# Optimization experiments

Hardware: AMD Instinct MI355X
Metric: run time of the kernel (lower is better)

Reference implementation:

```python
import jax, jax.numpy as jnp
import numpy as np

N = 20000      # nodes
E = 320000     # directed edges (before self-loops)
IN, HID, HEADS, OUT = 512, 256, 4, 256
NEG_SLOPE = 0.2  # PyG GATConv default


def setup_inputs() -> dict:
    key = jax.random.key(0)
    ks = jax.random.split(key, 10)
    x = jax.random.normal(ks[0], (N, IN), jnp.float32)
    edge_index = jax.random.randint(ks[1], (2, E), 0, N, jnp.int32)
    W1 = jax.random.normal(ks[2], (IN, HEADS * HID), jnp.float32) / np.sqrt(IN).astype(np.float32)
    att_src1 = jax.random.normal(ks[3], (HEADS, HID), jnp.float32) * 0.1
    att_dst1 = jax.random.normal(ks[4], (HEADS, HID), jnp.float32) * 0.1
    b1 = jnp.zeros((HEADS * HID,), jnp.float32)
    W2 = jax.random.normal(ks[5], (HEADS * HID, OUT), jnp.float32) / np.sqrt(HEADS * HID).astype(np.float32)
    att_src2 = jax.random.normal(ks[6], (1, OUT), jnp.float32) * 0.1
    att_dst2 = jax.random.normal(ks[7], (1, OUT), jnp.float32) * 0.1
    b2 = jnp.zeros((OUT,), jnp.float32)
    return {"x": x, "edge_index": edge_index, "W1": W1, "att_src1": att_src1,
            "att_dst1": att_dst1, "b1": b1, "W2": W2, "att_src2": att_src2,
            "att_dst2": att_dst2, "b2": b2}


def _segment_softmax(logits, seg, num_segments):
    # softmax over edges grouped by destination node (per head)
    m = jax.ops.segment_max(logits, seg, num_segments=num_segments)
    ex = jnp.exp(logits - m[seg])
    s = jax.ops.segment_sum(ex, seg, num_segments=num_segments)
    return ex / (s[seg] + 1e-16)


def _gat_conv(x, src, dst, W, att_src, att_dst, bias, heads, ch, num_nodes, concat):
    # PyG GATConv: h = W x (per head); alpha_e = softmax_dst(LeakyReLU(a_s.h_src + a_d.h_dst))
    h = (x @ W).reshape(num_nodes, heads, ch)          # [N,H,C]
    a_s = (h * att_src).sum(-1)                        # [N,H]
    a_d = (h * att_dst).sum(-1)                        # [N,H]
    logits = jax.nn.leaky_relu(a_s[src] + a_d[dst], NEG_SLOPE)   # [E,H]
    alpha = _segment_softmax(logits, dst, num_nodes)             # [E,H]
    msg = h[src] * alpha[:, :, None]                             # [E,H,C]
    out = jax.ops.segment_sum(msg, dst, num_segments=num_nodes)  # [N,H,C]
    out = out.reshape(num_nodes, heads * ch) if concat else out.mean(axis=1)
    return out + bias


def reference(x, edge_index, W1, att_src1, att_dst1, b1, W2, att_src2, att_dst2, b2):
    # add self-loops (PyG default add_self_loops=True)
    loop = jnp.arange(N, dtype=edge_index.dtype)
    src = jnp.concatenate([edge_index[0], loop])
    dst = jnp.concatenate([edge_index[1], loop])
    h = jax.nn.elu(_gat_conv(x, src, dst, W1, att_src1, att_dst1, b1, HEADS, HID, N, True))
    return _gat_conv(h, src, dst, W2, att_src2, att_dst2, b2, 1, OUT, N, False)
```

## Files before the change

kernel.cpp:

```cpp
#include <hip/hip_runtime.h>
#include <hip/hip_bf16.h>
#include <cfloat>
#include <math.h>

#define N_NODES 20000
#define M_PAD   20096
#define N_EDGES 320000
#define TOT_E   (N_EDGES + N_NODES)
#define EPAD    512
#define PS      (TOT_E + EPAD)
#define IN_F    512
#define HID     256
#define HEADS   4
#define OUT_F   256
#define H1DIM   (HEADS * HID)
#define NEG_SLOPE 0.2f

typedef __attribute__((ext_vector_type(8))) __bf16 bf16x8;
typedef __attribute__((ext_vector_type(4))) __bf16 bf16x4;
typedef __attribute__((ext_vector_type(4))) float f32x4;

__device__ __forceinline__ float lrelu(float x) { return x >= 0.f ? x : NEG_SLOPE * x; }
__device__ __forceinline__ float elu_lite(float x) { return x > 0.f ? x : __expf(x) - 1.f; }

__global__ void k_count(const int* __restrict__ ei, int* __restrict__ deg) {
  int e = blockIdx.x * 256 + threadIdx.x;
  if (e >= TOT_E) return;
  int dst = (e < N_EDGES) ? ei[N_EDGES + e] : (e - N_EDGES);
  atomicAdd(&deg[dst], 1);
}

__global__ void k_scan(const int* __restrict__ deg, int* __restrict__ off) {
  __shared__ int part[256];
  int tid = threadIdx.x;
  const int chunk = (N_NODES + 255) / 256;
  int s0 = tid * chunk;
  int s1 = s0 + chunk; if (s1 > N_NODES) s1 = N_NODES; if (s0 > N_NODES) s0 = N_NODES;
  int s = 0;
  for (int i = s0; i < s1; ++i) s += deg[i];
  part[tid] = s;
  __syncthreads();
  for (int d = 1; d < 256; d <<= 1) {
    int v = (tid >= d) ? part[tid - d] : 0;
    __syncthreads();
    part[tid] += v;
    __syncthreads();
  }
  int run = (tid == 0) ? 0 : part[tid - 1];
  for (int i = s0; i < s1; ++i) { off[i] = run; run += deg[i]; }
  if (tid == 255) off[N_NODES] = run;
}

__global__ void k_fill(const int* __restrict__ ei, const int* __restrict__ off,
                       int* __restrict__ cur, int* __restrict__ csr_src) {
  int e = blockIdx.x * 256 + threadIdx.x;
  if (e >= TOT_E) return;
  int src, dst;
  if (e < N_EDGES) { src = ei[e]; dst = ei[N_EDGES + e]; }
  else             { src = dst = e - N_EDGES; }
  int pos = atomicAdd(&cur[dst], 1);
  csr_src[off[dst] + pos] = src;
}

__global__ void k_f2b(const float* __restrict__ in, __bf16* __restrict__ out, int n4) {
  int i = blockIdx.x * 256 + threadIdx.x;
  if (i >= n4) return;
  float4 v = ((const float4*)in)[i];
  bf16x4 o = { (__bf16)v.x, (__bf16)v.y, (__bf16)v.z, (__bf16)v.w };
  ((bf16x4*)out)[i] = o;
}

__global__ void k_tr_f2b(const float* __restrict__ in, __bf16* __restrict__ out,
                         int R, int Cc) {
  __shared__ float tile[32][33];
  int c0 = blockIdx.x * 32, r0 = blockIdx.y * 32;
  int tx = threadIdx.x & 31, ty = threadIdx.x >> 5;
  for (int rr = ty; rr < 32; rr += 8)
    tile[rr][tx] = in[(size_t)(r0 + rr) * Cc + c0 + tx];
  __syncthreads();
  for (int rr = ty; rr < 32; rr += 8)
    out[(size_t)(c0 + rr) * R + r0 + tx] = (__bf16)tile[tx][rr];
}

__global__ __launch_bounds__(256) void k_gemm_bf16(
    const __bf16* __restrict__ A,
    const __bf16* __restrict__ Bt,
    __bf16* __restrict__ Cb,
    int M, int N, int K)
{
  __shared__ char lds[32768];
  char* As = lds;
  char* Bs = lds + 16384;

  const int t = threadIdx.x;
  const int lane = t & 63;
  const int wid = t >> 6;
  const int wm = wid >> 1, wn = wid & 1;
  const int row0 = blockIdx.y * 128;
  const int col0 = blockIdx.x * 128;

  f32x4 acc[4][4];
#pragma unroll
  for (int i = 0; i < 4; ++i)
#pragma unroll
    for (int j = 0; j < 4; ++j) acc[i][j] = (f32x4){0.f, 0.f, 0.f, 0.f};

  for (int k0 = 0; k0 < K; k0 += 64) {
#pragma unroll
    for (int i = 0; i < 4; ++i) {
      int j = i * 256 + t;
      int r = j >> 3;
      int cc = (j & 7) ^ (r & 7);
      const __bf16* gp = A + (size_t)(row0 + r) * K + k0 + cc * 8;
      __builtin_amdgcn_global_load_lds(
          (const __attribute__((address_space(1))) void*)gp,
          (__attribute__((address_space(3))) void*)(As + j * 16), 16, 0, 0);
    }
#pragma unroll
    for (int i = 0; i < 4; ++i) {
      int j = i * 256 + t;
      int r = j >> 3;
      int cc = (j & 7) ^ (r & 7);
      const __bf16* gp = Bt + (size_t)(col0 + r) * K + k0 + cc * 8;
      __builtin_amdgcn_global_load_lds(
          (const __attribute__((address_space(1))) void*)gp,
          (__attribute__((address_space(3))) void*)(Bs + j * 16), 16, 0, 0);
    }
    __syncthreads();

#pragma unroll
    for (int ks = 0; ks < 2; ++ks) {
      bf16x8 af[4], bfr[4];
#pragma unroll
      for (int i = 0; i < 4; ++i) {
        int rA = wm * 64 + i * 16 + (lane & 15);
        int chA = (ks * 4 + (lane >> 4)) ^ (rA & 7);
        af[i] = *(const bf16x8*)(As + rA * 128 + chA * 16);
        int rB = wn * 64 + i * 16 + (lane & 15);
        int chB = (ks * 4 + (lane >> 4)) ^ (rB & 7);
        bfr[i] = *(const bf16x8*)(Bs + rB * 128 + chB * 16);
      }
#pragma unroll
      for (int i = 0; i < 4; ++i)
#pragma unroll
        for (int jn = 0; jn < 4; ++jn)
          acc[i][jn] = __builtin_amdgcn_mfma_f32_16x16x32_bf16(
              af[i], bfr[jn], acc[i][jn], 0, 0, 0);
    }
    __syncthreads();
  }

#pragma unroll
  for (int i = 0; i < 4; ++i) {
    int growb = row0 + wm * 64 + i * 16 + (lane >> 4) * 4;
#pragma unroll
    for (int jn = 0; jn < 4; ++jn) {
      int gcol = col0 + wn * 64 + jn * 16 + (lane & 15);
#pragma unroll
      for (int r = 0; r < 4; ++r) {
        int grow = growb + r;
        if (grow < M) Cb[(size_t)grow * N + gcol] = (__bf16)acc[i][jn][r];
      }
    }
  }
}

__global__ void k_attn1(const __bf16* __restrict__ h1b, const float* __restrict__ att_s,
                        const float* __restrict__ att_d, float* __restrict__ as,
                        float* __restrict__ ad) {
  int n = blockIdx.x;
  int t = threadIdx.x;
  int head = t >> 6, lane = t & 63;
  bf16x4 hv = *(const bf16x4*)(h1b + (size_t)n * H1DIM + t * 4);
  float4 sv = *(const float4*)(att_s + t * 4);
  float4 dv = *(const float4*)(att_d + t * 4);
  float h0 = (float)hv[0], h1 = (float)hv[1], h2 = (float)hv[2], h3 = (float)hv[3];
  float ss = h0 * sv.x + h1 * sv.y + h2 * sv.z + h3 * sv.w;
  float sd = h0 * dv.x + h1 * dv.y + h2 * dv.z + h3 * dv.w;
#pragma unroll
  for (int d = 32; d; d >>= 1) { ss += __shfl_xor(ss, d); sd += __shfl_xor(sd, d); }
  if (lane == 0) { as[n * HEADS + head] = ss; ad[n * HEADS + head] = sd; }
}

__global__ void k_attn2(const __bf16* __restrict__ h2b, const float* __restrict__ att_s,
                        const float* __restrict__ att_d, float* __restrict__ as,
                        float* __restrict__ ad) {
  int n = blockIdx.x;
  int lane = threadIdx.x;
  bf16x4 hv = *(const bf16x4*)(h2b + (size_t)n * OUT_F + lane * 4);
  float4 sv = *(const float4*)(att_s + lane * 4);
  float4 dv = *(const float4*)(att_d + lane * 4);
  float h0 = (float)hv[0], h1 = (float)hv[1], h2 = (float)hv[2], h3 = (float)hv[3];
  float ss = h0 * sv.x + h1 * sv.y + h2 * sv.z + h3 * sv.w;
  float sd = h0 * dv.x + h1 * dv.y + h2 * dv.z + h3 * dv.w;
#pragma unroll
  for (int d = 32; d; d >>= 1) { ss += __shfl_xor(ss, d); sd += __shfl_xor(sd, d); }
  if (lane == 0) { as[n] = ss; ad[n] = sd; }
}

__global__ void k_w1(const int* __restrict__ off, const int* __restrict__ csr,
                     const float* __restrict__ as, const float* __restrict__ ad,
                     float* __restrict__ wnP, float* __restrict__ inv) {
  int n = blockIdx.x;
  int lane = threadIdx.x;
  int beg = off[n], end = off[n + 1];
  float4 adv = *(const float4*)&ad[n * 4];
  float p0 = 0.f, p1 = 0.f, p2 = 0.f, p3 = 0.f;
  for (int p = beg + lane; p < end; p += 64) {
    int s = csr[p];
    float4 av = *(const float4*)&as[s * 4];
    float w0 = __expf(lrelu(av.x + adv.x));
    float w1 = __expf(lrelu(av.y + adv.y));
    float w2 = __expf(lrelu(av.z + adv.z));
    float w3 = __expf(lrelu(av.w + adv.w));
    p0 += w0; p1 += w1; p2 += w2; p3 += w3;
    wnP[p] = w0;
    wnP[PS + p] = w1;
    wnP[2 * PS + p] = w2;
    wnP[3 * PS + p] = w3;
  }
#pragma unroll
  for (int d = 32; d; d >>= 1) {
    p0 += __shfl_xor(p0, d); p1 += __shfl_xor(p1, d);
    p2 += __shfl_xor(p2, d); p3 += __shfl_xor(p3, d);
  }
  if (lane == 0) {
    float4 iv = {1.f / (p0 + 1e-16f), 1.f / (p1 + 1e-16f),
                 1.f / (p2 + 1e-16f), 1.f / (p3 + 1e-16f)};
    *(float4*)&inv[n * 4] = iv;
  }
}

__global__ void k_w2(const int* __restrict__ off, const int* __restrict__ csr,
                     const float* __restrict__ as, const float* __restrict__ ad,
                     float* __restrict__ wn, float* __restrict__ inv) {
  int n = blockIdx.x;
  int lane = threadIdx.x;
  int beg = off[n], end = off[n + 1];
  float adv = ad[n];
  float ps = 0.f;
  for (int p = beg + lane; p < end; p += 64) {
    int s = csr[p];
    float w = __expf(lrelu(as[s] + adv));
    wn[p] = w;
    ps += w;
  }
#pragma unroll
  for (int d = 32; d; d >>= 1) ps += __shfl_xor(ps, d);
  if (lane == 0) inv[n] = 1.f / (ps + 1e-16f);
}

__global__ __launch_bounds__(256) void k_gather1(
    const int* __restrict__ off, const int* __restrict__ csr,
    const __bf16* __restrict__ h1b, const float* __restrict__ wnP,
    const float* __restrict__ inv, const float* __restrict__ b1,
    __bf16* __restrict__ heluB) {
  int bid = blockIdx.x;
  int slice = bid & 7;
  int head = slice >> 1;
  int cb = slice * 128;
  int w = threadIdx.x >> 6, lane = threadIdx.x & 63;
  int g = lane >> 4;
  int cg = lane & 15;
  int n = (bid >> 3) * 16 + w * 4 + g;
  int beg = off[n], end = off[n + 1];
  int deg = end - beg;
  int itmax = deg;
  itmax = max(itmax, __shfl_xor(itmax, 16));
  itmax = max(itmax, __shfl_xor(itmax, 32));

  float acc[8] = {0.f, 0.f, 0.f, 0.f, 0.f, 0.f, 0.f, 0.f};
  const __bf16* hb = h1b + cb + cg * 8;
  const float* wp = wnP + (size_t)head * PS;
#pragma unroll 2
  for (int i = 0; i < itmax; ++i) {
    int e = beg + i;
    bool v = (i < deg);
    int s = v ? csr[e] : 0;
    float wv = v ? wp[e] : 0.f;
    uint4 u = *(const uint4*)(hb + (size_t)s * H1DIM);
    acc[0] = fmaf(wv, __uint_as_float(u.x << 16), acc[0]);
    acc[1] = fmaf(wv, __uint_as_float(u.x & 0xffff0000u), acc[1]);
    acc[2] = fmaf(wv, __uint_as_float(u.y << 16), acc[2]);
    acc[3] = fmaf(wv, __uint_as_float(u.y & 0xffff0000u), acc[3]);
    acc[4] = fmaf(wv, __uint_as_float(u.z << 16), acc[4]);
    acc[5] = fmaf(wv, __uint_as_float(u.z & 0xffff0000u), acc[5]);
    acc[6] = fmaf(wv, __uint_as_float(u.w << 16), acc[6]);
    acc[7] = fmaf(wv, __uint_as_float(u.w & 0xffff0000u), acc[7]);
  }

  float iv = inv[n * 4 + head];
  float4 bv0 = *(const float4*)(b1 + cb + cg * 8);
  float4 bv1 = *(const float4*)(b1 + cb + cg * 8 + 4);
  float bb[8] = {bv0.x, bv0.y, bv0.z, bv0.w, bv1.x, bv1.y, bv1.z, bv1.w};
  bf16x8 o;
#pragma unroll
  for (int k = 0; k < 8; ++k) {
    float v = acc[k] * iv + bb[k];
    o[k] = (__bf16)elu_lite(v);
  }
  *(bf16x8*)(heluB + (size_t)n * H1DIM + cb + cg * 8) = o;
}

__global__ __launch_bounds__(256) void k_gather2(
    const int* __restrict__ off, const int* __restrict__ csr,
    const __bf16* __restrict__ h2b, const float* __restrict__ wn,
    const float* __restrict__ inv, const float* __restrict__ b2,
    float* __restrict__ out) {
  int bid = blockIdx.x;
  int slice = bid & 3;
  int cb = slice * 64;
  int w = threadIdx.x >> 6, lane = threadIdx.x & 63;
  int g = lane >> 3;
  int cg = lane & 7;
  int n = (bid >> 2) * 32 + w * 8 + g;
  int beg = off[n], end = off[n + 1];
  int deg = end - beg;
  int itmax = deg;
  itmax = max(itmax, __shfl_xor(itmax, 8));
  itmax = max(itmax, __shfl_xor(itmax, 16));
  itmax = max(itmax, __shfl_xor(itmax, 32));

  float acc[8] = {0.f, 0.f, 0.f, 0.f, 0.f, 0.f, 0.f, 0.f};
  const __bf16* hb = h2b + cb + cg * 8;
#pragma unroll 2
  for (int i = 0; i < itmax; ++i) {
    int e = beg + i;
    bool v = (i < deg);
    int s = v ? csr[e] : 0;
    float wv = v ? wn[e] : 0.f;
    uint4 u = *(const uint4*)(hb + (size_t)s * OUT_F);
    acc[0] = fmaf(wv, __uint_as_float(u.x << 16), acc[0]);
    acc[1] = fmaf(wv, __uint_as_float(u.x & 0xffff0000u), acc[1]);
    acc[2] = fmaf(wv, __uint_as_float(u.y << 16), acc[2]);
    acc[3] = fmaf(wv, __uint_as_float(u.y & 0xffff0000u), acc[3]);
    acc[4] = fmaf(wv, __uint_as_float(u.z << 16), acc[4]);
    acc[5] = fmaf(wv, __uint_as_float(u.z & 0xffff0000u), acc[5]);
    acc[6] = fmaf(wv, __uint_as_float(u.w << 16), acc[6]);
    acc[7] = fmaf(wv, __uint_as_float(u.w & 0xffff0000u), acc[7]);
  }

  float iv = inv[n];
  float4 bv0 = *(const float4*)(b2 + cb + cg * 8);
  float4 bv1 = *(const float4*)(b2 + cb + cg * 8 + 4);
  float* op = out + (size_t)n * OUT_F + cb + cg * 8;
  float4 o0 = {acc[0] * iv + bv0.x, acc[1] * iv + bv0.y,
               acc[2] * iv + bv0.z, acc[3] * iv + bv0.w};
  float4 o1 = {acc[4] * iv + bv1.x, acc[5] * iv + bv1.y,
               acc[6] * iv + bv1.z, acc[7] * iv + bv1.w};
  *(float4*)op = o0;
  *(float4*)(op + 4) = o1;
}

extern "C" void kernel_launch(void* const* d_in, const int* in_sizes, int n_in,
                              void* d_out, int out_size, void* d_ws, size_t ws_size,
                              hipStream_t stream) {
  const float* x      = (const float*)d_in[0];
  const int*   ei     = (const int*)d_in[1];
  const float* W1     = (const float*)d_in[2];
  const float* att_s1 = (const float*)d_in[3];
  const float* att_d1 = (const float*)d_in[4];
  const float* b1     = (const float*)d_in[5];
  const float* W2     = (const float*)d_in[6];
  const float* att_s2 = (const float*)d_in[7];
  const float* att_d2 = (const float*)d_in[8];
  const float* b2     = (const float*)d_in[9];
  float* out = (float*)d_out;

  char* w = (char*)d_ws;
  auto alloc = [&](size_t bytes) {
    char* p = w;
    w += (bytes + 255) & ~(size_t)255;
    return p;
  };
  int*    deg   = (int*)alloc((size_t)N_NODES * 4);
  int*    off   = (int*)alloc((size_t)(N_NODES + 1) * 4);
  int*    cur   = (int*)alloc((size_t)N_NODES * 4);
  int*    csr   = (int*)alloc((size_t)PS * 4);
  float*  as1   = (float*)alloc((size_t)N_NODES * HEADS * 4);
  float*  ad1   = (float*)alloc((size_t)N_NODES * HEADS * 4);
  float*  as2   = (float*)alloc((size_t)N_NODES * 4);
  float*  ad2   = (float*)alloc((size_t)N_NODES * 4);
  float*  wnP   = (float*)alloc((size_t)PS * HEADS * 4);
  float*  inv1  = (float*)alloc((size_t)N_NODES * HEADS * 4);
  float*  wn2   = (float*)alloc((size_t)PS * 4);
  float*  inv2  = (float*)alloc((size_t)N_NODES * 4);
  __bf16* xb    = (__bf16*)alloc((size_t)M_PAD * IN_F * 2);
  __bf16* w1t   = (__bf16*)alloc((size_t)H1DIM * IN_F * 2);
  __bf16* w2t   = (__bf16*)alloc((size_t)OUT_F * H1DIM * 2);
  __bf16* h1b   = (__bf16*)alloc((size_t)M_PAD * H1DIM * 2);
  __bf16* heluB = (__bf16*)alloc((size_t)M_PAD * H1DIM * 2);
  __bf16* h2b   = (__bf16*)alloc((size_t)M_PAD * OUT_F * 2);
  if ((size_t)(w - (char*)d_ws) > ws_size) return;

  hipMemsetAsync(deg, 0, (size_t)N_NODES * 4, stream);
  hipMemsetAsync(cur, 0, (size_t)N_NODES * 4, stream);
  hipMemsetAsync(csr + TOT_E, 0, (size_t)EPAD * 4, stream);

  k_count<<<(TOT_E + 255) / 256, 256, 0, stream>>>(ei, deg);
  k_scan<<<1, 256, 0, stream>>>(deg, off);
  k_fill<<<(TOT_E + 255) / 256, 256, 0, stream>>>(ei, off, cur, csr);

  int n4 = N_NODES * IN_F / 4;
  k_f2b<<<(n4 + 255) / 256, 256, 0, stream>>>(x, xb, n4);
  k_tr_f2b<<<dim3(H1DIM / 32, IN_F / 32), 256, 0, stream>>>(W1, w1t, IN_F, H1DIM);
  k_tr_f2b<<<dim3(OUT_F / 32, H1DIM / 32), 256, 0, stream>>>(W2, w2t, H1DIM, OUT_F);

  k_gemm_bf16<<<dim3(H1DIM / 128, M_PAD / 128), 256, 0, stream>>>(
      xb, w1t, h1b, N_NODES, H1DIM, IN_F);
  k_attn1<<<N_NODES, 256, 0, stream>>>(h1b, att_s1, att_d1, as1, ad1);
  k_w1<<<N_NODES, 64, 0, stream>>>(off, csr, as1, ad1, wnP, inv1);
  k_gather1<<<(N_NODES / 16) * 8, 256, 0, stream>>>(off, csr, h1b, wnP, inv1, b1, heluB);

  k_gemm_bf16<<<dim3(OUT_F / 128, M_PAD / 128), 256, 0, stream>>>(
      heluB, w2t, h2b, N_NODES, OUT_F, H1DIM);
  k_attn2<<<N_NODES, 64, 0, stream>>>(h2b, att_s2, att_d2, as2, ad2);
  k_w2<<<N_NODES, 64, 0, stream>>>(off, csr, as2, ad2, wn2, inv2);
  k_gather2<<<(N_NODES / 32) * 4, 256, 0, stream>>>(off, csr, h2b, wn2, inv2, b2, out);
}
```

Measured before the change: 303.6 us.

## Fuse attention-logit dot products into GEMM epilogue and split edges across gather lanes

```diff
diff --git a/kernel.cpp b/kernel.cpp
--- a/kernel.cpp
+++ b/kernel.cpp
@@ -86,6 +86,8 @@
     const __bf16* __restrict__ A,
     const __bf16* __restrict__ Bt,
     __bf16* __restrict__ Cb,
+    const float* __restrict__ attS, const float* __restrict__ attD,
+    float* __restrict__ asO, float* __restrict__ adO, int hstride,
     int M, int N, int K)
 {
   __shared__ char lds[32768];
@@ -163,39 +165,39 @@
       }
     }
   }
-}
-
-__global__ void k_attn1(const __bf16* __restrict__ h1b, const float* __restrict__ att_s,
-                        const float* __restrict__ att_d, float* __restrict__ as,
-                        float* __restrict__ ad) {
-  int n = blockIdx.x;
-  int t = threadIdx.x;
-  int head = t >> 6, lane = t & 63;
-  bf16x4 hv = *(const bf16x4*)(h1b + (size_t)n * H1DIM + t * 4);
-  float4 sv = *(const float4*)(att_s + t * 4);
-  float4 dv = *(const float4*)(att_d + t * 4);
-  float h0 = (float)hv[0], h1 = (float)hv[1], h2 = (float)hv[2], h3 = (float)hv[3];
-  float ss = h0 * sv.x + h1 * sv.y + h2 * sv.z + h3 * sv.w;
-  float sd = h0 * dv.x + h1 * dv.y + h2 * dv.z + h3 * dv.w;
-#pragma unroll
-  for (int d = 32; d; d >>= 1) { ss += __shfl_xor(ss, d); sd += __shfl_xor(sd, d); }
-  if (lane == 0) { as[n * HEADS + head] = ss; ad[n * HEADS + head] = sd; }
-}
-
-__global__ void k_attn2(const __bf16* __restrict__ h2b, const float* __restrict__ att_s,
-                        const float* __restrict__ att_d, float* __restrict__ as,
-                        float* __restrict__ ad) {
-  int n = blockIdx.x;
-  int lane = threadIdx.x;
-  bf16x4 hv = *(const bf16x4*)(h2b + (size_t)n * OUT_F + lane * 4);
-  float4 sv = *(const float4*)(att_s + lane * 4);
-  float4 dv = *(const float4*)(att_d + lane * 4);
-  float h0 = (float)hv[0], h1 = (float)hv[1], h2 = (float)hv[2], h3 = (float)hv[3];
-  float ss = h0 * sv.x + h1 * sv.y + h2 * sv.z + h3 * sv.w;
-  float sd = h0 * dv.x + h1 * dv.y + h2 * dv.z + h3 * dv.w;
-#pragma unroll
-  for (int d = 32; d; d >>= 1) { ss += __shfl_xor(ss, d); sd += __shfl_xor(sd, d); }
-  if (lane == 0) { as[n] = ss; ad[n] = sd; }
+
+  int head = (col0 + wn * 64) >> 8;
+  float sv[4], dv[4];
+#pragma unroll
+  for (int jn = 0; jn < 4; ++jn) {
+    int c = col0 + wn * 64 + jn * 16 + (lane & 15);
+    sv[jn] = attS[c];
+    dv[jn] = attD[c];
+  }
+#pragma unroll
+  for (int i = 0; i < 4; ++i) {
+#pragma unroll
+    for (int r = 0; r < 4; ++r) {
+      float pa = 0.f, pd = 0.f;
+#pragma unroll
+      for (int jn = 0; jn < 4; ++jn) {
+        pa = fmaf(acc[i][jn][r], sv[jn], pa);
+        pd = fmaf(acc[i][jn][r], dv[jn], pd);
+      }
+#pragma unroll
+      for (int d = 1; d < 16; d <<= 1) {
+        pa += __shfl_xor(pa, d);
+        pd += __shfl_xor(pd, d);
+      }
+      if ((lane & 15) == 0) {
+        int grow = row0 + wm * 64 + i * 16 + (lane >> 4) * 4 + r;
+        if (grow < M) {
+          atomicAdd(&asO[(size_t)grow * hstride + head], pa);
+          atomicAdd(&adO[(size_t)grow * hstride + head], pd);
+        }
+      }
+    }
+  }
 }
 
 __global__ void k_w1(const int* __restrict__ off, const int* __restrict__ csr,
@@ -260,22 +262,20 @@
   int head = slice >> 1;
   int cb = slice * 128;
   int w = threadIdx.x >> 6, lane = threadIdx.x & 63;
-  int g = lane >> 4;
+  int sub = lane >> 4;
   int cg = lane & 15;
-  int n = (bid >> 3) * 16 + w * 4 + g;
+  int n = (bid >> 3) * 4 + w;
   int beg = off[n], end = off[n + 1];
   int deg = end - beg;
-  int itmax = deg;
-  itmax = max(itmax, __shfl_xor(itmax, 16));
-  itmax = max(itmax, __shfl_xor(itmax, 32));
+  int it = (deg + 3) >> 2;
 
   float acc[8] = {0.f, 0.f, 0.f, 0.f, 0.f, 0.f, 0.f, 0.f};
   const __bf16* hb = h1b + cb + cg * 8;
   const float* wp = wnP + (size_t)head * PS;
 #pragma unroll 2
-  for (int i = 0; i < itmax; ++i) {
-    int e = beg + i;
-    bool v = (i < deg);
+  for (int i = 0; i < it; ++i) {
+    int e = beg + i * 4 + sub;
+    bool v = (e < end);
     int s = v ? csr[e] : 0;
     float wv = v ? wp[e] : 0.f;
     uint4 u = *(const uint4*)(hb + (size_t)s * H1DIM);
@@ -288,18 +288,24 @@
     acc[6] = fmaf(wv, __uint_as_float(u.w << 16), acc[6]);
     acc[7] = fmaf(wv, __uint_as_float(u.w & 0xffff0000u), acc[7]);
   }
-
-  float iv = inv[n * 4 + head];
-  float4 bv0 = *(const float4*)(b1 + cb + cg * 8);
-  float4 bv1 = *(const float4*)(b1 + cb + cg * 8 + 4);
-  float bb[8] = {bv0.x, bv0.y, bv0.z, bv0.w, bv1.x, bv1.y, bv1.z, bv1.w};
-  bf16x8 o;
 #pragma unroll
   for (int k = 0; k < 8; ++k) {
-    float v = acc[k] * iv + bb[k];
-    o[k] = (__bf16)elu_lite(v);
-  }
-  *(bf16x8*)(heluB + (size_t)n * H1DIM + cb + cg * 8) = o;
+    acc[k] += __shfl_xor(acc[k], 16);
+    acc[k] += __shfl_xor(acc[k], 32);
+  }
+  if (sub == 0) {
+    float iv = inv[n * 4 + head];
+    float4 bv0 = *(const float4*)(b1 + cb + cg * 8);
+    float4 bv1 = *(const float4*)(b1 + cb + cg * 8 + 4);
+    float bb[8] = {bv0.x, bv0.y, bv0.z, bv0.w, bv1.x, bv1.y, bv1.z, bv1.w};
+    bf16x8 o;
+#pragma unroll
+    for (int k = 0; k < 8; ++k) {
+      float v = acc[k] * iv + bb[k];
+      o[k] = (__bf16)elu_lite(v);
+    }
+    *(bf16x8*)(heluB + (size_t)n * H1DIM + cb + cg * 8) = o;
+  }
 }
 
 __global__ __launch_bounds__(256) void k_gather2(
@@ -311,22 +317,19 @@
   int slice = bid & 3;
   int cb = slice * 64;
   int w = threadIdx.x >> 6, lane = threadIdx.x & 63;
-  int g = lane >> 3;
+  int sub = lane >> 3;
   int cg = lane & 7;
-  int n = (bid >> 2) * 32 + w * 8 + g;
+  int n = (bid >> 2) * 4 + w;
   int beg = off[n], end = off[n + 1];
   int deg = end - beg;
-  int itmax = deg;
-  itmax = max(itmax, __shfl_xor(itmax, 8));
-  itmax = max(itmax, __shfl_xor(itmax, 16));
-  itmax = max(itmax, __shfl_xor(itmax, 32));
+  int it = (deg + 7) >> 3;
 
   float acc[8] = {0.f, 0.f, 0.f, 0.f, 0.f, 0.f, 0.f, 0.f};
   const __bf16* hb = h2b + cb + cg * 8;
 #pragma unroll 2
-  for (int i = 0; i < itmax; ++i) {
-    int e = beg + i;
-    bool v = (i < deg);
+  for (int i = 0; i < it; ++i) {
+    int e = beg + i * 8 + sub;
+    bool v = (e < end);
     int s = v ? csr[e] : 0;
     float wv = v ? wn[e] : 0.f;
     uint4 u = *(const uint4*)(hb + (size_t)s * OUT_F);
@@ -339,17 +342,24 @@
     acc[6] = fmaf(wv, __uint_as_float(u.w << 16), acc[6]);
     acc[7] = fmaf(wv, __uint_as_float(u.w & 0xffff0000u), acc[7]);
   }
-
-  float iv = inv[n];
-  float4 bv0 = *(const float4*)(b2 + cb + cg * 8);
-  float4 bv1 = *(const float4*)(b2 + cb + cg * 8 + 4);
-  float* op = out + (size_t)n * OUT_F + cb + cg * 8;
-  float4 o0 = {acc[0] * iv + bv0.x, acc[1] * iv + bv0.y,
-               acc[2] * iv + bv0.z, acc[3] * iv + bv0.w};
-  float4 o1 = {acc[4] * iv + bv1.x, acc[5] * iv + bv1.y,
-               acc[6] * iv + bv1.z, acc[7] * iv + bv1.w};
-  *(float4*)op = o0;
-  *(float4*)(op + 4) = o1;
+#pragma unroll
+  for (int k = 0; k < 8; ++k) {
+    acc[k] += __shfl_xor(acc[k], 8);
+    acc[k] += __shfl_xor(acc[k], 16);
+    acc[k] += __shfl_xor(acc[k], 32);
+  }
+  if (sub == 0) {
+    float iv = inv[n];
+    float4 bv0 = *(const float4*)(b2 + cb + cg * 8);
+    float4 bv1 = *(const float4*)(b2 + cb + cg * 8 + 4);
+    float* op = out + (size_t)n * OUT_F + cb + cg * 8;
+    float4 o0 = {acc[0] * iv + bv0.x, acc[1] * iv + bv0.y,
+                 acc[2] * iv + bv0.z, acc[3] * iv + bv0.w};
+    float4 o1 = {acc[4] * iv + bv1.x, acc[5] * iv + bv1.y,
+                 acc[6] * iv + bv1.z, acc[7] * iv + bv1.w};
+    *(float4*)op = o0;
+    *(float4*)(op + 4) = o1;
+  }
 }
 
 extern "C" void kernel_launch(void* const* d_in, const int* in_sizes, int n_in,
@@ -396,6 +406,10 @@
   hipMemsetAsync(deg, 0, (size_t)N_NODES * 4, stream);
   hipMemsetAsync(cur, 0, (size_t)N_NODES * 4, stream);
   hipMemsetAsync(csr + TOT_E, 0, (size_t)EPAD * 4, stream);
+  hipMemsetAsync(as1, 0, (size_t)N_NODES * HEADS * 4, stream);
+  hipMemsetAsync(ad1, 0, (size_t)N_NODES * HEADS * 4, stream);
+  hipMemsetAsync(as2, 0, (size_t)N_NODES * 4, stream);
+  hipMemsetAsync(ad2, 0, (size_t)N_NODES * 4, stream);
 
   k_count<<<(TOT_E + 255) / 256, 256, 0, stream>>>(ei, deg);
   k_scan<<<1, 256, 0, stream>>>(deg, off);
@@ -407,14 +421,12 @@
   k_tr_f2b<<<dim3(OUT_F / 32, H1DIM / 32), 256, 0, stream>>>(W2, w2t, H1DIM, OUT_F);
 
   k_gemm_bf16<<<dim3(H1DIM / 128, M_PAD / 128), 256, 0, stream>>>(
-      xb, w1t, h1b, N_NODES, H1DIM, IN_F);
-  k_attn1<<<N_NODES, 256, 0, stream>>>(h1b, att_s1, att_d1, as1, ad1);
+      xb, w1t, h1b, att_s1, att_d1, as1, ad1, HEADS, N_NODES, H1DIM, IN_F);
   k_w1<<<N_NODES, 64, 0, stream>>>(off, csr, as1, ad1, wnP, inv1);
-  k_gather1<<<(N_NODES / 16) * 8, 256, 0, stream>>>(off, csr, h1b, wnP, inv1, b1, heluB);
+  k_gather1<<<(N_NODES / 4) * 8, 256, 0, stream>>>(off, csr, h1b, wnP, inv1, b1, heluB);
 
   k_gemm_bf16<<<dim3(OUT_F / 128, M_PAD / 128), 256, 0, stream>>>(
-      heluB, w2t, h2b, N_NODES, OUT_F, H1DIM);
-  k_attn2<<<N_NODES, 64, 0, stream>>>(h2b, att_s2, att_d2, as2, ad2);
+      heluB, w2t, h2b, att_s2, att_d2, as2, ad2, 1, N_NODES, OUT_F, H1DIM);
   k_w2<<<N_NODES, 64, 0, stream>>>(off, csr, as2, ad2, wn2, inv2);
-  k_gather2<<<(N_NODES / 32) * 4, 256, 0, stream>>>(off, csr, h2b, wn2, inv2, b2, out);
-}
+  k_gather2<<<(N_NODES / 4) * 4, 256, 0, stream>>>(off, csr, h2b, wn2, inv2, b2, out);
+}
```

New measurement: 342.5 us. +12.8%, slower.

## Switch to fp16 storage with packed half2 gather accumulation and prenormalized weights

Applied to the files above, without the earlier changes.

```diff
diff --git a/kernel.cpp b/kernel.cpp
--- a/kernel.cpp
+++ b/kernel.cpp
@@ -1,5 +1,5 @@
 #include <hip/hip_runtime.h>
-#include <hip/hip_bf16.h>
+#include <hip/hip_fp16.h>
 #include <cfloat>
 #include <math.h>
 
@@ -16,8 +16,8 @@
 #define H1DIM   (HEADS * HID)
 #define NEG_SLOPE 0.2f
 
-typedef __attribute__((ext_vector_type(8))) __bf16 bf16x8;
-typedef __attribute__((ext_vector_type(4))) __bf16 bf16x4;
+typedef __attribute__((ext_vector_type(8))) _Float16 f16x8;
+typedef __attribute__((ext_vector_type(4))) _Float16 f16x4;
 typedef __attribute__((ext_vector_type(4))) float f32x4;
 
 __device__ __forceinline__ float lrelu(float x) { return x >= 0.f ? x : NEG_SLOPE * x; }
@@ -62,15 +62,15 @@
   csr_src[off[dst] + pos] = src;
 }
 
-__global__ void k_f2b(const float* __restrict__ in, __bf16* __restrict__ out, int n4) {
+__global__ void k_f2h(const float* __restrict__ in, _Float16* __restrict__ out, int n4) {
   int i = blockIdx.x * 256 + threadIdx.x;
   if (i >= n4) return;
   float4 v = ((const float4*)in)[i];
-  bf16x4 o = { (__bf16)v.x, (__bf16)v.y, (__bf16)v.z, (__bf16)v.w };
-  ((bf16x4*)out)[i] = o;
-}
-
-__global__ void k_tr_f2b(const float* __restrict__ in, __bf16* __restrict__ out,
+  f16x4 o = { (_Float16)v.x, (_Float16)v.y, (_Float16)v.z, (_Float16)v.w };
+  ((f16x4*)out)[i] = o;
+}
+
+__global__ void k_tr_f2h(const float* __restrict__ in, _Float16* __restrict__ out,
                          int R, int Cc) {
   __shared__ float tile[32][33];
   int c0 = blockIdx.x * 32, r0 = blockIdx.y * 32;
@@ -79,13 +79,13 @@
     tile[rr][tx] = in[(size_t)(r0 + rr) * Cc + c0 + tx];
   __syncthreads();
   for (int rr = ty; rr < 32; rr += 8)
-    out[(size_t)(c0 + rr) * R + r0 + tx] = (__bf16)tile[tx][rr];
-}
-
-__global__ __launch_bounds__(256) void k_gemm_bf16(
-    const __bf16* __restrict__ A,
-    const __bf16* __restrict__ Bt,
-    __bf16* __restrict__ Cb,
+    out[(size_t)(c0 + rr) * R + r0 + tx] = (_Float16)tile[tx][rr];
+}
+
+__global__ __launch_bounds__(256) void k_gemm_f16(
+    const _Float16* __restrict__ A,
+    const _Float16* __restrict__ Bt,
+    _Float16* __restrict__ Ch,
     int M, int N, int K)
 {
   __shared__ char lds[32768];
@@ -111,7 +111,7 @@
       int j = i * 256 + t;
       int r = j >> 3;
       int cc = (j & 7) ^ (r & 7);
-      const __bf16* gp = A + (size_t)(row0 + r) * K + k0 + cc * 8;
+      const _Float16* gp = A + (size_t)(row0 + r) * K + k0 + cc * 8;
       __builtin_amdgcn_global_load_lds(
           (const __attribute__((address_space(1))) void*)gp,
           (__attribute__((address_space(3))) void*)(As + j * 16), 16, 0, 0);
@@ -121,7 +121,7 @@
       int j = i * 256 + t;
       int r = j >> 3;
       int cc = (j & 7) ^ (r & 7);
-      const __bf16* gp = Bt + (size_t)(col0 + r) * K + k0 + cc * 8;
+      const _Float16* gp = Bt + (size_t)(col0 + r) * K + k0 + cc * 8;
       __builtin_amdgcn_global_load_lds(
           (const __attribute__((address_space(1))) void*)gp,
           (__attribute__((address_space(3))) void*)(Bs + j * 16), 16, 0, 0);
@@ -130,21 +130,21 @@
 
 #pragma unroll
     for (int ks = 0; ks < 2; ++ks) {
-      bf16x8 af[4], bfr[4];
+      f16x8 af[4], bfr[4];
 #pragma unroll
       for (int i = 0; i < 4; ++i) {
         int rA = wm * 64 + i * 16 + (lane & 15);
         int chA = (ks * 4 + (lane >> 4)) ^ (rA & 7);
-        af[i] = *(const bf16x8*)(As + rA * 128 + chA * 16);
+        af[i] = *(const f16x8*)(As + rA * 128 + chA * 16);
         int rB = wn * 64 + i * 16 + (lane & 15);
         int chB = (ks * 4 + (lane >> 4)) ^ (rB & 7);
-        bfr[i] = *(const bf16x8*)(Bs + rB * 128 + chB * 16);
+        bfr[i] = *(const f16x8*)(Bs + rB * 128 + chB * 16);
       }
 #pragma unroll
       for (int i = 0; i < 4; ++i)
 #pragma unroll
         for (int jn = 0; jn < 4; ++jn)
-          acc[i][jn] = __builtin_amdgcn_mfma_f32_16x16x32_bf16(
+          acc[i][jn] = __builtin_amdgcn_mfma_f32_16x16x32_f16(
               af[i], bfr[jn], acc[i][jn], 0, 0, 0);
     }
     __syncthreads();
@@ -159,19 +159,19 @@
 #pragma unroll
       for (int r = 0; r < 4; ++r) {
         int grow = growb + r;
-        if (grow < M) Cb[(size_t)grow * N + gcol] = (__bf16)acc[i][jn][r];
+        if (grow < M) Ch[(size_t)grow * N + gcol] = (_Float16)acc[i][jn][r];
       }
     }
   }
 }
 
-__global__ void k_attn1(const __bf16* __restrict__ h1b, const float* __restrict__ att_s,
+__global__ void k_attn1(const _Float16* __restrict__ h1h, const float* __restrict__ att_s,
                         const float* __restrict__ att_d, float* __restrict__ as,
                         float* __restrict__ ad) {
   int n = blockIdx.x;
   int t = threadIdx.x;
   int head = t >> 6, lane = t & 63;
-  bf16x4 hv = *(const bf16x4*)(h1b + (size_t)n * H1DIM + t * 4);
+  f16x4 hv = *(const f16x4*)(h1h + (size_t)n * H1DIM + t * 4);
   float4 sv = *(const float4*)(att_s + t * 4);
   float4 dv = *(const float4*)(att_d + t * 4);
   float h0 = (float)hv[0], h1 = (float)hv[1], h2 = (float)hv[2], h3 = (float)hv[3];
@@ -182,12 +182,12 @@
   if (lane == 0) { as[n * HEADS + head] = ss; ad[n * HEADS + head] = sd; }
 }
 
-__global__ void k_attn2(const __bf16* __restrict__ h2b, const float* __restrict__ att_s,
+__global__ void k_attn2(const _Float16* __restrict__ h2h, const float* __restrict__ att_s,
                         const float* __restrict__ att_d, float* __restrict__ as,
                         float* __restrict__ ad) {
   int n = blockIdx.x;
   int lane = threadIdx.x;
-  bf16x4 hv = *(const bf16x4*)(h2b + (size_t)n * OUT_F + lane * 4);
+  f16x4 hv = *(const f16x4*)(h2h + (size_t)n * OUT_F + lane * 4);
   float4 sv = *(const float4*)(att_s + lane * 4);
   float4 dv = *(const float4*)(att_d + lane * 4);
   float h0 = (float)hv[0], h1 = (float)hv[1], h2 = (float)hv[2], h3 = (float)hv[3];
@@ -200,7 +200,7 @@
 
 __global__ void k_w1(const int* __restrict__ off, const int* __restrict__ csr,
                      const float* __restrict__ as, const float* __restrict__ ad,
-                     float* __restrict__ wnP, float* __restrict__ inv) {
+                     float* __restrict__ wnP, __half* __restrict__ wnH) {
   int n = blockIdx.x;
   int lane = threadIdx.x;
   int beg = off[n], end = off[n + 1];
@@ -224,16 +224,19 @@
     p0 += __shfl_xor(p0, d); p1 += __shfl_xor(p1, d);
     p2 += __shfl_xor(p2, d); p3 += __shfl_xor(p3, d);
   }
-  if (lane == 0) {
-    float4 iv = {1.f / (p0 + 1e-16f), 1.f / (p1 + 1e-16f),
-                 1.f / (p2 + 1e-16f), 1.f / (p3 + 1e-16f)};
-    *(float4*)&inv[n * 4] = iv;
+  float i0 = 1.f / (p0 + 1e-16f), i1 = 1.f / (p1 + 1e-16f);
+  float i2 = 1.f / (p2 + 1e-16f), i3 = 1.f / (p3 + 1e-16f);
+  for (int p = beg + lane; p < end; p += 64) {
+    wnH[p]          = __float2half_rn(wnP[p] * i0);
+    wnH[PS + p]     = __float2half_rn(wnP[PS + p] * i1);
+    wnH[2 * PS + p] = __float2half_rn(wnP[2 * PS + p] * i2);
+    wnH[3 * PS + p] = __float2half_rn(wnP[3 * PS + p] * i3);
   }
 }
 
 __global__ void k_w2(const int* __restrict__ off, const int* __restrict__ csr,
                      const float* __restrict__ as, const float* __restrict__ ad,
-                     float* __restrict__ wn, float* __restrict__ inv) {
+                     float* __restrict__ wnP, __half* __restrict__ wnH) {
   int n = blockIdx.x;
   int lane = threadIdx.x;
   int beg = off[n], end = off[n + 1];
@@ -242,19 +245,20 @@
   for (int p = beg + lane; p < end; p += 64) {
     int s = csr[p];
     float w = __expf(lrelu(as[s] + adv));
-    wn[p] = w;
+    wnP[p] = w;
     ps += w;
   }
 #pragma unroll
   for (int d = 32; d; d >>= 1) ps += __shfl_xor(ps, d);
-  if (lane == 0) inv[n] = 1.f / (ps + 1e-16f);
+  float iv = 1.f / (ps + 1e-16f);
+  for (int p = beg + lane; p < end; p += 64)
+    wnH[p] = __float2half_rn(wnP[p] * iv);
 }
 
 __global__ __launch_bounds__(256) void k_gather1(
     const int* __restrict__ off, const int* __restrict__ csr,
-    const __bf16* __restrict__ h1b, const float* __restrict__ wnP,
-    const float* __restrict__ inv, const float* __restrict__ b1,
-    __bf16* __restrict__ heluB) {
+    const _Float16* __restrict__ h1h, const __half* __restrict__ wnH,
+    const float* __restrict__ b1, _Float16* __restrict__ heluH) {
   int bid = blockIdx.x;
   int slice = bid & 7;
   int head = slice >> 1;
@@ -269,44 +273,42 @@
   itmax = max(itmax, __shfl_xor(itmax, 16));
   itmax = max(itmax, __shfl_xor(itmax, 32));
 
-  float acc[8] = {0.f, 0.f, 0.f, 0.f, 0.f, 0.f, 0.f, 0.f};
-  const __bf16* hb = h1b + cb + cg * 8;
-  const float* wp = wnP + (size_t)head * PS;
+  __half2 a0 = __float2half2_rn(0.f), a1 = a0, a2 = a0, a3 = a0;
+  const _Float16* hb = h1h + cb + cg * 8;
+  const __half* wp = wnH + (size_t)head * PS;
+  const __half hz = __float2half_rn(0.f);
 #pragma unroll 2
   for (int i = 0; i < itmax; ++i) {
     int e = beg + i;
     bool v = (i < deg);
     int s = v ? csr[e] : 0;
-    float wv = v ? wp[e] : 0.f;
+    __half wv = v ? wp[e] : hz;
+    __half2 w2 = __half2half2(wv);
     uint4 u = *(const uint4*)(hb + (size_t)s * H1DIM);
-    acc[0] = fmaf(wv, __uint_as_float(u.x << 16), acc[0]);
-    acc[1] = fmaf(wv, __uint_as_float(u.x & 0xffff0000u), acc[1]);
-    acc[2] = fmaf(wv, __uint_as_float(u.y << 16), acc[2]);
-    acc[3] = fmaf(wv, __uint_as_float(u.y & 0xffff0000u), acc[3]);
-    acc[4] = fmaf(wv, __uint_as_float(u.z << 16), acc[4]);
-    acc[5] = fmaf(wv, __uint_as_float(u.z & 0xffff0000u), acc[5]);
-    acc[6] = fmaf(wv, __uint_as_float(u.w << 16), acc[6]);
-    acc[7] = fmaf(wv, __uint_as_float(u.w & 0xffff0000u), acc[7]);
-  }
-
-  float iv = inv[n * 4 + head];
+    a0 = __hfma2(w2, *(__half2*)&u.x, a0);
+    a1 = __hfma2(w2, *(__half2*)&u.y, a1);
+    a2 = __hfma2(w2, *(__half2*)&u.z, a2);
+    a3 = __hfma2(w2, *(__half2*)&u.w, a3);
+  }
+
+  float vv[8] = { __low2float(a0), __high2float(a0), __low2float(a1), __high2float(a1),
+                  __low2float(a2), __high2float(a2), __low2float(a3), __high2float(a3) };
   float4 bv0 = *(const float4*)(b1 + cb + cg * 8);
   float4 bv1 = *(const float4*)(b1 + cb + cg * 8 + 4);
   float bb[8] = {bv0.x, bv0.y, bv0.z, bv0.w, bv1.x, bv1.y, bv1.z, bv1.w};
-  bf16x8 o;
+  f16x8 o;
 #pragma unroll
   for (int k = 0; k < 8; ++k) {
-    float v = acc[k] * iv + bb[k];
-    o[k] = (__bf16)elu_lite(v);
-  }
-  *(bf16x8*)(heluB + (size_t)n * H1DIM + cb + cg * 8) = o;
+    float v = vv[k] + bb[k];
+    o[k] = (_Float16)elu_lite(v);
+  }
+  *(f16x8*)(heluH + (size_t)n * H1DIM + cb + cg * 8) = o;
 }
 
 __global__ __launch_bounds__(256) void k_gather2(
     const int* __restrict__ off, const int* __restrict__ csr,
-    const __bf16* __restrict__ h2b, const float* __restrict__ wn,
-    const float* __restrict__ inv, const float* __restrict__ b2,
-    float* __restrict__ out) {
+    const _Float16* __restrict__ h2h, const __half* __restrict__ wnH,
+    const float* __restrict__ b2, float* __restrict__ out) {
   int bid = blockIdx.x;
   int slice = bid & 3;
   int cb = slice * 64;
@@ -321,33 +323,30 @@
   itmax = max(itmax, __shfl_xor(itmax, 16));
   itmax = max(itmax, __shfl_xor(itmax, 32));
 
-  float acc[8] = {0.f, 0.f, 0.f, 0.f, 0.f, 0.f, 0.f, 0.f};
-  const __bf16* hb = h2b + cb + cg * 8;
+  __half2 a0 = __float2half2_rn(0.f), a1 = a0, a2 = a0, a3 = a0;
+  const _Float16* hb = h2h + cb + cg * 8;
+  const __half hz = __float2half_rn(0.f);
 #pragma unroll 2
   for (int i = 0; i < itmax; ++i) {
     int e = beg + i;
     bool v = (i < deg);
     int s = v ? csr[e] : 0;
-    float wv = v ? wn[e] : 0.f;
+    __half wv = v ? wnH[e] : hz;
+    __half2 w2 = __half2half2(wv);
     uint4 u = *(const uint4*)(hb + (size_t)s * OUT_F);
-    acc[0] = fmaf(wv, __uint_as_float(u.x << 16), acc[0]);
-    acc[1] = fmaf(wv, __uint_as_float(u.x & 0xffff0000u), acc[1]);
-    acc[2] = fmaf(wv, __uint_as_float(u.y << 16), acc[2]);
-    acc[3] = fmaf(wv, __uint_as_float(u.y & 0xffff0000u), acc[3]);
-    acc[4] = fmaf(wv, __uint_as_float(u.z << 16), acc[4]);
-    acc[5] = fmaf(wv, __uint_as_float(u.z & 0xffff0000u), acc[5]);
-    acc[6] = fmaf(wv, __uint_as_float(u.w << 16), acc[6]);
-    acc[7] = fmaf(wv, __uint_as_float(u.w & 0xffff0000u), acc[7]);
-  }
-
-  float iv = inv[n];
+    a0 = __hfma2(w2, *(__half2*)&u.x, a0);
+    a1 = __hfma2(w2, *(__half2*)&u.y, a1);
+    a2 = __hfma2(w2, *(__half2*)&u.z, a2);
+    a3 = __hfma2(w2, *(__half2*)&u.w, a3);
+  }
+
   float4 bv0 = *(const float4*)(b2 + cb + cg * 8);
   float4 bv1 = *(const float4*)(b2 + cb + cg * 8 + 4);
   float* op = out + (size_t)n * OUT_F + cb + cg * 8;
-  float4 o0 = {acc[0] * iv + bv0.x, acc[1] * iv + bv0.y,
-               acc[2] * iv + bv0.z, acc[3] * iv + bv0.w};
-  float4 o1 = {acc[4] * iv + bv1.x, acc[5] * iv + bv1.y,
-               acc[6] * iv + bv1.z, acc[7] * iv + bv1.w};
+  float4 o0 = { __low2float(a0) + bv0.x, __high2float(a0) + bv0.y,
+                __low2float(a1) + bv0.z, __high2float(a1) + bv0.w };
+  float4 o1 = { __low2float(a2) + bv1.x, __high2float(a2) + bv1.y,
+                __low2float(a3) + bv1.z, __high2float(a3) + bv1.w };
   *(float4*)op = o0;
   *(float4*)(op + 4) = o1;
 }
@@ -373,24 +372,24 @@
     w += (bytes + 255) & ~(size_t)255;
     return p;
   };
-  int*    deg   = (int*)alloc((size_t)N_NODES * 4);
-  int*    off   = (int*)alloc((size_t)(N_NODES + 1) * 4);
-  int*    cur   = (int*)alloc((size_t)N_NODES * 4);
-  int*    csr   = (int*)alloc((size_t)PS * 4);
-  float*  as1   = (float*)alloc((size_t)N_NODES * HEADS * 4);
-  float*  ad1   = (float*)alloc((size_t)N_NODES * HEADS * 4);
-  float*  as2   = (float*)alloc((size_t)N_NODES * 4);
-  float*  ad2   = (float*)alloc((size_t)N_NODES * 4);
-  float*  wnP   = (float*)alloc((size_t)PS * HEADS * 4);
-  float*  inv1  = (float*)alloc((size_t)N_NODES * HEADS * 4);
-  float*  wn2   = (float*)alloc((size_t)PS * 4);
-  float*  inv2  = (float*)alloc((size_t)N_NODES * 4);
-  __bf16* xb    = (__bf16*)alloc((size_t)M_PAD * IN_F * 2);
-  __bf16* w1t   = (__bf16*)alloc((size_t)H1DIM * IN_F * 2);
-  __bf16* w2t   = (__bf16*)alloc((size_t)OUT_F * H1DIM * 2);
-  __bf16* h1b   = (__bf16*)alloc((size_t)M_PAD * H1DIM * 2);
-  __bf16* heluB = (__bf16*)alloc((size_t)M_PAD * H1DIM * 2);
-  __bf16* h2b   = (__bf16*)alloc((size_t)M_PAD * OUT_F * 2);
+  int*       deg   = (int*)alloc((size_t)N_NODES * 4);
+  int*       off   = (int*)alloc((size_t)(N_NODES + 1) * 4);
+  int*       cur   = (int*)alloc((size_t)N_NODES * 4);
+  int*       csr   = (int*)alloc((size_t)PS * 4);
+  float*     as1   = (float*)alloc((size_t)N_NODES * HEADS * 4);
+  float*     ad1   = (float*)alloc((size_t)N_NODES * HEADS * 4);
+  float*     as2   = (float*)alloc((size_t)N_NODES * 4);
+  float*     ad2   = (float*)alloc((size_t)N_NODES * 4);
+  float*     wnP   = (float*)alloc((size_t)PS * HEADS * 4);
+  __half*    wnH   = (__half*)alloc((size_t)PS * HEADS * 2);
+  float*     wn2P  = (float*)alloc((size_t)PS * 4);
+  __half*    wn2H  = (__half*)alloc((size_t)PS * 2);
+  _Float16*  xh    = (_Float16*)alloc((size_t)M_PAD * IN_F * 2);
+  _Float16*  w1t   = (_Float16*)alloc((size_t)H1DIM * IN_F * 2);
+  _Float16*  w2t   = (_Float16*)alloc((size_t)OUT_F * H1DIM * 2);
+  _Float16*  h1h   = (_Float16*)alloc((size_t)M_PAD * H1DIM * 2);
+  _Float16*  heluH = (_Float16*)alloc((size_t)M_PAD * H1DIM * 2);
+  _Float16*  h2h   = (_Float16*)alloc((size_t)M_PAD * OUT_F * 2);
   if ((size_t)(w - (char*)d_ws) > ws_size) return;
 
   hipMemsetAsync(deg, 0, (size_t)N_NODES * 4, stream);
@@ -402,19 +401,19 @@
   k_fill<<<(TOT_E + 255) / 256, 256, 0, stream>>>(ei, off, cur, csr);
 
   int n4 = N_NODES * IN_F / 4;
-  k_f2b<<<(n4 + 255) / 256, 256, 0, stream>>>(x, xb, n4);
-  k_tr_f2b<<<dim3(H1DIM / 32, IN_F / 32), 256, 0, stream>>>(W1, w1t, IN_F, H1DIM);
-  k_tr_f2b<<<dim3(OUT_F / 32, H1DIM / 32), 256, 0, stream>>>(W2, w2t, H1DIM, OUT_F);
-
-  k_gemm_bf16<<<dim3(H1DIM / 128, M_PAD / 128), 256, 0, stream>>>(
-      xb, w1t, h1b, N_NODES, H1DIM, IN_F);
-  k_attn1<<<N_NODES, 256, 0, stream>>>(h1b, att_s1, att_d1, as1, ad1);
-  k_w1<<<N_NODES, 64, 0, stream>>>(off, csr, as1, ad1, wnP, inv1);
-  k_gather1<<<(N_NODES / 16) * 8, 256, 0, stream>>>(off, csr, h1b, wnP, inv1, b1, heluB);
-
-  k_gemm_bf16<<<dim3(OUT_F / 128, M_PAD / 128), 256, 0, stream>>>(
-      heluB, w2t, h2b, N_NODES, OUT_F, H1DIM);
-  k_attn2<<<N_NODES, 64, 0, stream>>>(h2b, att_s2, att_d2, as2, ad2);
-  k_w2<<<N_NODES, 64, 0, stream>>>(off, csr, as2, ad2, wn2, inv2);
-  k_gather2<<<(N_NODES / 32) * 4, 256, 0, stream>>>(off, csr, h2b, wn2, inv2, b2, out);
-}
+  k_f2h<<<(n4 + 255) / 256, 256, 0, stream>>>(x, xh, n4);
+  k_tr_f2h<<<dim3(H1DIM / 32, IN_F / 32), 256, 0, stream>>>(W1, w1t, IN_F, H1DIM);
+  k_tr_f2h<<<dim3(OUT_F / 32, H1DIM / 32), 256, 0, stream>>>(W2, w2t, H1DIM, OUT_F);
+
+  k_gemm_f16<<<dim3(H1DIM / 128, M_PAD / 128), 256, 0, stream>>>(
+      xh, w1t, h1h, N_NODES, H1DIM, IN_F);
+  k_attn1<<<N_NODES, 256, 0, stream>>>(h1h, att_s1, att_d1, as1, ad1);
+  k_w1<<<N_NODES, 64, 0, stream>>>(off, csr, as1, ad1, wnP, wnH);
+  k_gather1<<<(N_NODES / 16) * 8, 256, 0, stream>>>(off, csr, h1h, wnH, b1, heluH);
+
+  k_gemm_f16<<<dim3(OUT_F / 128, M_PAD / 128), 256, 0, stream>>>(
+      heluH, w2t, h2h, N_NODES, OUT_F, H1DIM);
+  k_attn2<<<N_NODES, 64, 0, stream>>>(h2h, att_s2, att_d2, as2, ad2);
+  k_w2<<<N_NODES, 64, 0, stream>>>(off, csr, as2, ad2, wn2P, wn2H);
+  k_gather2<<<(N_NODES / 32) * 4, 256, 0, stream>>>(off, csr, h2h, wn2H, b2, out);
+}
```

Result: slower. 340.0 us (+12.0%).
